# Kernel tuning notes

Hardware: AMD Instinct MI355X
Metric: run time of the kernel (lower is better)

## Reference

```python
import jax, jax.numpy as jnp
import numpy as np

N_NODES = 50000


def _gcn_conv(x, src, dst, W, b, n):
    # PyG GCNConv: h = x @ W; symmetric normalization with self-loops; scatter-add; + bias
    h = x @ W
    deg = jax.ops.segment_sum(jnp.ones_like(dst, dtype=h.dtype), dst, num_segments=n)
    dinv = jax.lax.rsqrt(jnp.maximum(deg, 1.0))  # self-loops guarantee deg >= 1
    norm = dinv[src] * dinv[dst]                 # [E_total]
    msgs = h[src] * norm[:, None]                # gather + scale
    out = jax.ops.segment_sum(msgs, dst, num_segments=n)
    return out + b


def setup_inputs() -> dict:
    key = jax.random.key(0)
    k1, k2, k3, k4 = jax.random.split(key, 4)
    d, f = 128, 128
    x = jax.random.normal(k1, (N_NODES, d), dtype=jnp.float32)
    edge_index = jax.random.randint(k2, (2, 800000), 0, N_NODES, dtype=jnp.int64)
    W1 = jax.random.normal(k3, (d, f), dtype=jnp.float32) / np.sqrt(d)
    b1 = jnp.zeros((f,), dtype=jnp.float32)
    W2 = jax.random.normal(k4, (f, 1), dtype=jnp.float32) / np.sqrt(f)
    b2 = jnp.zeros((1,), dtype=jnp.float32)
    return {"x": x, "edge_index": edge_index, "W1": W1, "b1": b1, "W2": W2, "b2": b2}


def reference(x, edge_index, W1, b1, W2, b2):
    n = x.shape[0]
    loops = jnp.arange(n, dtype=edge_index.dtype)
    src = jnp.concatenate([edge_index[0], loops])
    dst = jnp.concatenate([edge_index[1], loops])
    h = _gcn_conv(x, src, dst, W1, b1, n)
    h = jax.nn.relu(h)
    out = _gcn_conv(h, src, dst, W2, b2, n)
    return out
```

## Files before the change

### kernel.cpp

```cpp
#include <hip/hip_runtime.h>
#include <hip/hip_fp16.h>

#define D 128
#define BINW 128
#define BINCAP 4096
#define BINA_BLOCKS 512

typedef _Float16 half8 __attribute__((ext_vector_type(8)));
typedef float float4v __attribute__((ext_vector_type(4)));

__global__ void detect_kernel(const int* __restrict__ idx, int* __restrict__ flag) {
  if (threadIdx.x == 0 && blockIdx.x == 0) {
    int any = 0;
    for (int i = 0; i < 64; ++i) any |= idx[2 * i + 1];
    *flag = (any == 0) ? 1 : 0;
  }
}

__global__ __launch_bounds__(256) void bin_scatter_kernel(const int* __restrict__ idx,
                                                          const int* __restrict__ flagp,
                                                          int* __restrict__ binCount,
                                                          unsigned* __restrict__ binned,
                                                          int E, int nbin) {
  __shared__ int hist[512];
  __shared__ int cur[512];
  const int t = threadIdx.x;
  for (int b = t; b < 512; b += 256) hist[b] = 0;
  __syncthreads();
  const int is64 = *flagp;
  const int chunk = (E + gridDim.x - 1) / gridDim.x;
  const int lo = blockIdx.x * chunk;
  const int hi = min(lo + chunk, E);
  for (int e = lo + t; e < hi; e += 256) {
    int d = is64 ? idx[2 * (E + e)] : idx[E + e];
    atomicAdd(&hist[d >> 7], 1);
  }
  __syncthreads();
  for (int b = t; b < nbin; b += 256) {
    int hv = hist[b];
    cur[b] = hv ? atomicAdd(&binCount[b], hv) : 0;
  }
  __syncthreads();
  for (int e = lo + t; e < hi; e += 256) {
    int s, d;
    if (is64) { s = idx[2 * e]; d = idx[2 * (E + e)]; }
    else      { s = idx[e];     d = idx[E + e]; }
    int b = d >> 7;
    int pos = atomicAdd(&cur[b], 1);
    pos = min(pos, BINCAP - 1);
    binned[(size_t)b * BINCAP + pos] = (unsigned)s | ((unsigned)(d & 127) << 16);
  }
}

__global__ __launch_bounds__(256) void bin_sort_kernel(const int* __restrict__ binCount,
                                                       const unsigned* __restrict__ binned,
                                                       unsigned short* __restrict__ csr,
                                                       int* __restrict__ rowptr,
                                                       int* __restrict__ rend,
                                                       float* __restrict__ dinv,
                                                       int n, int nbin) {
  __shared__ unsigned rec[BINCAP];
  __shared__ unsigned short srt[BINCAP];
  __shared__ int hist[BINW];
  __shared__ int scn[BINW];
  __shared__ int cur[BINW];
  const int t = threadIdx.x;
  const int b = blockIdx.x;
  int cnt = binCount[b];
  if (cnt > BINCAP) cnt = BINCAP;
  const size_t gbase = (size_t)b * BINCAP;

  for (int i = t; i < cnt; i += 256) rec[i] = binned[gbase + i];
  if (t < BINW) hist[t] = 0;
  __syncthreads();
  for (int i = t; i < cnt; i += 256) atomicAdd(&hist[rec[i] >> 16], 1);
  __syncthreads();
  if (t < BINW) scn[t] = hist[t];
  __syncthreads();
  for (int off = 1; off < BINW; off <<= 1) {
    int u = 0;
    if (t < BINW && t >= off) u = scn[t - off];
    __syncthreads();
    if (t < BINW) scn[t] += u;
    __syncthreads();
  }
  if (t < BINW) cur[t] = scn[t] - hist[t];
  __syncthreads();
  for (int i = t; i < cnt; i += 256) {
    unsigned r = rec[i];
    int pos = atomicAdd(&cur[r >> 16], 1);
    srt[pos] = (unsigned short)(r & 0xFFFFu);
  }
  __syncthreads();
  const unsigned* srt32 = (const unsigned*)srt;
  unsigned* csr32 = (unsigned*)(csr + gbase);
  for (int i = t; i < (cnt + 1) / 2; i += 256) csr32[i] = srt32[i];

  const int node = b * BINW + t;
  if (t < BINW && node < n) {
    int deg = hist[t];
    int start = (int)gbase + (scn[t] - deg);
    rowptr[node] = start;
    rend[node]   = start + deg;
    dinv[node]   = rsqrtf((float)(deg + 1));
  }
}

__global__ __launch_bounds__(256) void gemm1_mfma_kernel(const float* __restrict__ x,
                                                         const float* __restrict__ W,
                                                         __half* __restrict__ h, int n) {
  __shared__ uint4 bfrag[8][4][64];
  const int t = threadIdx.x;

  for (int e = t; e < 2048; e += 256) {
    const int nt = e >> 8;
    const int kk = (e >> 6) & 3;
    const int L  = e & 63;
    const int nn = nt * 16 + (L & 15);
    const int k0 = kk * 32 + (L >> 4) * 8;
    half8 v;
#pragma unroll
    for (int j = 0; j < 8; ++j) v[j] = (_Float16)W[(k0 + j) * D + nn];
    bfrag[nt][kk][L] = *(uint4*)&v;
  }
  __syncthreads();

  const int wave = t >> 6;
  const int lane = t & 63;
  const int r0 = blockIdx.x * 64 + wave * 16;
  if (r0 >= n) return;

  const int mrow = r0 + (lane & 15);
  const int mc = (mrow < n) ? mrow : (n - 1);
  half8 af[4];
#pragma unroll
  for (int kk = 0; kk < 4; ++kk) {
    const float* xp = x + (size_t)mc * D + kk * 32 + (lane >> 4) * 8;
    float4 lo = *(const float4*)xp;
    float4 hi = *(const float4*)(xp + 4);
    half8 v;
    v[0] = (_Float16)lo.x; v[1] = (_Float16)lo.y;
    v[2] = (_Float16)lo.z; v[3] = (_Float16)lo.w;
    v[4] = (_Float16)hi.x; v[5] = (_Float16)hi.y;
    v[6] = (_Float16)hi.z; v[7] = (_Float16)hi.w;
    af[kk] = v;
  }

  float4v acc[8];
#pragma unroll
  for (int nt = 0; nt < 8; ++nt) acc[nt] = (float4v){0.f, 0.f, 0.f, 0.f};

#pragma unroll
  for (int nt = 0; nt < 8; ++nt) {
    uint4 b0 = bfrag[nt][0][lane];
    uint4 b1 = bfrag[nt][1][lane];
    uint4 b2 = bfrag[nt][2][lane];
    uint4 b3 = bfrag[nt][3][lane];
    acc[nt] = __builtin_amdgcn_mfma_f32_16x16x32_f16(af[0], *(half8*)&b0, acc[nt], 0, 0, 0);
    acc[nt] = __builtin_amdgcn_mfma_f32_16x16x32_f16(af[1], *(half8*)&b1, acc[nt], 0, 0, 0);
    acc[nt] = __builtin_amdgcn_mfma_f32_16x16x32_f16(af[2], *(half8*)&b2, acc[nt], 0, 0, 0);
    acc[nt] = __builtin_amdgcn_mfma_f32_16x16x32_f16(af[3], *(half8*)&b3, acc[nt], 0, 0, 0);
  }

  const int rbase = r0 + (lane >> 4) * 4;
  const int col = lane & 15;
#pragma unroll
  for (int r = 0; r < 4; ++r) {
    const int rr = rbase + r;
    if (rr < n) {
      __half* hp = h + (size_t)rr * D + col;
#pragma unroll
      for (int nt = 0; nt < 8; ++nt) hp[nt * 16] = __float2half(acc[nt][r]);
    }
  }
}

__device__ __forceinline__ void unpack8(uint4 p, float f[8]) {
  float2 t;
  t = __half22float2(*(__half2*)&p.x); f[0] = t.x; f[1] = t.y;
  t = __half22float2(*(__half2*)&p.y); f[2] = t.x; f[3] = t.y;
  t = __half22float2(*(__half2*)&p.z); f[4] = t.x; f[5] = t.y;
  t = __half22float2(*(__half2*)&p.w); f[6] = t.x; f[7] = t.y;
}

__global__ __launch_bounds__(256) void gather1_kernel(const __half* __restrict__ h,
                                                      const int* __restrict__ rowptr,
                                                      const int* __restrict__ rend,
                                                      const unsigned short* __restrict__ csr,
                                                      const float* __restrict__ dinv,
                                                      const float* __restrict__ b1,
                                                      const float* __restrict__ W2,
                                                      float* __restrict__ zw, int n) {
  const int node = blockIdx.x * 4 + (threadIdx.x >> 6);
  if (node >= n) return;
  const int lane = threadIdx.x & 63;
  const int q    = lane >> 4;
  const int fb   = (lane & 15) * 8;

  const float di = dinv[node];
  float a[8] = {0.f, 0.f, 0.f, 0.f, 0.f, 0.f, 0.f, 0.f};
  if (q == 0) {
    uint4 p = *(const uint4*)(h + (size_t)node * D + fb);
    float f[8]; unpack8(p, f);
    float s2 = di * di;
#pragma unroll
    for (int k = 0; k < 8; ++k) a[k] = f[k] * s2;
  }

  const int end = rend[node];
  int j = rowptr[node] + q;
  while (j + 4 < end) {
    int s0 = csr[j];
    int s1 = csr[j + 4];
    uint4 p0 = *(const uint4*)(h + (size_t)s0 * D + fb);
    uint4 p1 = *(const uint4*)(h + (size_t)s1 * D + fb);
    float w0 = di * dinv[s0];
    float w1 = di * dinv[s1];
    float f0[8], f1[8]; unpack8(p0, f0); unpack8(p1, f1);
#pragma unroll
    for (int k = 0; k < 8; ++k) a[k] = fmaf(f0[k], w0, a[k]);
#pragma unroll
    for (int k = 0; k < 8; ++k) a[k] = fmaf(f1[k], w1, a[k]);
    j += 8;
  }
  if (j < end) {
    int s0 = csr[j];
    uint4 p0 = *(const uint4*)(h + (size_t)s0 * D + fb);
    float w0 = di * dinv[s0];
    float f0[8]; unpack8(p0, f0);
#pragma unroll
    for (int k = 0; k < 8; ++k) a[k] = fmaf(f0[k], w0, a[k]);
  }

#pragma unroll
  for (int k = 0; k < 8; ++k) {
    a[k] += __shfl_xor(a[k], 16, 64);
    a[k] += __shfl_xor(a[k], 32, 64);
  }

  float4 blo = *(const float4*)(b1 + fb);
  float4 bhi = *(const float4*)(b1 + fb + 4);
  float4 wlo = *(const float4*)(W2 + fb);
  float4 whi = *(const float4*)(W2 + fb + 4);
  float bb[8] = {blo.x, blo.y, blo.z, blo.w, bhi.x, bhi.y, bhi.z, bhi.w};
  float ww[8] = {wlo.x, wlo.y, wlo.z, wlo.w, whi.x, whi.y, whi.z, whi.w};
  float p = 0.f;
#pragma unroll
  for (int k = 0; k < 8; ++k) p += fmaxf(a[k] + bb[k], 0.f) * ww[k];
#pragma unroll
  for (int off = 8; off > 0; off >>= 1) p += __shfl_xor(p, off, 64);
  if (lane == 0) zw[node] = p * di;
}

__global__ void gather2_kernel(const float* __restrict__ zw,
                               const float* __restrict__ dinv,
                               const int* __restrict__ rowptr,
                               const int* __restrict__ rend,
                               const unsigned short* __restrict__ csr,
                               const float* __restrict__ b2,
                               float* __restrict__ out, int n) {
  int i = blockIdx.x * blockDim.x + threadIdx.x;
  if (i >= n) return;
  float s = zw[i];
  const int lo = rowptr[i], hi = rend[i];
  for (int j = lo; j < hi; ++j) s += zw[csr[j]];
  out[i] = s * dinv[i] + b2[0];
}

extern "C" void kernel_launch(void* const* d_in, const int* in_sizes, int n_in,
                              void* d_out, int out_size, void* d_ws, size_t ws_size,
                              hipStream_t stream) {
  const float* x   = (const float*)d_in[0];
  const int*   idx = (const int*)d_in[1];
  const float* W1  = (const float*)d_in[2];
  const float* b1  = (const float*)d_in[3];
  const float* W2  = (const float*)d_in[4];
  const float* b2  = (const float*)d_in[5];
  float* out = (float*)d_out;

  const int n = in_sizes[0] / D;
  const int E = in_sizes[1] / 2;
  const int nbin = (n + BINW - 1) / BINW;

  char* ws = (char*)d_ws;
  size_t off = 0;
  auto carve = [&](size_t bytes) { char* p = ws + off; off += (bytes + 255) & ~(size_t)255; return p; };
  int*            flag     = (int*)carve(4);
  int*            binCount = (int*)carve((size_t)nbin * 4);
  unsigned*       binned   = (unsigned*)carve((size_t)nbin * BINCAP * 4);
  unsigned short* csr      = (unsigned short*)carve((size_t)nbin * BINCAP * 2);
  int*            rowptr   = (int*)carve((size_t)n * 4);
  int*            rend     = (int*)carve((size_t)n * 4);
  float*          dinv     = (float*)carve((size_t)n * 4);
  __half*         h        = (__half*)carve((size_t)n * D * 2);
  float*          zw       = (float*)carve((size_t)n * 4);

  detect_kernel<<<1, 64, 0, stream>>>(idx, flag);
  hipMemsetAsync(binCount, 0, (size_t)nbin * 4, stream);
  bin_scatter_kernel<<<BINA_BLOCKS, 256, 0, stream>>>(idx, flag, binCount, binned, E, nbin);
  bin_sort_kernel<<<nbin, 256, 0, stream>>>(binCount, binned, csr, rowptr, rend, dinv, n, nbin);
  gemm1_mfma_kernel<<<(n + 63) / 64, 256, 0, stream>>>(x, W1, h, n);
  gather1_kernel<<<(n + 3) / 4, 256, 0, stream>>>(h, rowptr, rend, csr, dinv, b1, W2, zw, n);
  gather2_kernel<<<(n + 255) / 256, 256, 0, stream>>>(zw, dinv, rowptr, rend, csr, b2, out, n);
}
```

Before: 161.5 us.

## Fold index-width detection into scatter, stage GEMM output, unroll gathers deeper

Removes the separate detect kernel launch: each scatter block now works out the int32/int64 index width itself by reading the first 64 entries. The GEMM stages its fp16 output tile through shared memory so global stores become coalesced 16-byte writes instead of scattered 2-byte ones. The layer-1 gather loop now issues four independent neighbor row loads per iteration instead of two, using predicated dummy loads for the tail. The layer-2 gather is unrolled by four. In exchange, every scatter block repeats the detection reads, the GEMM gains two barriers, and the gather uses more registers.

```diff
diff --git a/kernel.cpp b/kernel.cpp
--- a/kernel.cpp
+++ b/kernel.cpp
@@ -9,25 +9,22 @@
 typedef _Float16 half8 __attribute__((ext_vector_type(8)));
 typedef float float4v __attribute__((ext_vector_type(4)));
 
-__global__ void detect_kernel(const int* __restrict__ idx, int* __restrict__ flag) {
-  if (threadIdx.x == 0 && blockIdx.x == 0) {
-    int any = 0;
-    for (int i = 0; i < 64; ++i) any |= idx[2 * i + 1];
-    *flag = (any == 0) ? 1 : 0;
-  }
-}
-
 __global__ __launch_bounds__(256) void bin_scatter_kernel(const int* __restrict__ idx,
-                                                          const int* __restrict__ flagp,
                                                           int* __restrict__ binCount,
                                                           unsigned* __restrict__ binned,
                                                           int E, int nbin) {
   __shared__ int hist[512];
   __shared__ int cur[512];
+  __shared__ int s_is64;
   const int t = threadIdx.x;
   for (int b = t; b < 512; b += 256) hist[b] = 0;
-  __syncthreads();
-  const int is64 = *flagp;
+  if (t == 0) {
+    int any = 0;
+    for (int i = 0; i < 64; ++i) any |= idx[2 * i + 1];
+    s_is64 = (any == 0) ? 1 : 0;
+  }
+  __syncthreads();
+  const int is64 = s_is64;
   const int chunk = (E + gridDim.x - 1) / gridDim.x;
   const int lo = blockIdx.x * chunk;
   const int hi = min(lo + chunk, E);
@@ -109,7 +106,8 @@
 __global__ __launch_bounds__(256) void gemm1_mfma_kernel(const float* __restrict__ x,
                                                          const float* __restrict__ W,
                                                          __half* __restrict__ h, int n) {
-  __shared__ uint4 bfrag[8][4][64];
+  __shared__ uint4 smem[2048];
+  uint4 (*bfrag)[4][64] = (uint4(*)[4][64])smem;
   const int t = threadIdx.x;
 
   for (int e = t; e < 2048; e += 256) {
@@ -128,7 +126,6 @@
   const int wave = t >> 6;
   const int lane = t & 63;
   const int r0 = blockIdx.x * 64 + wave * 16;
-  if (r0 >= n) return;
 
   const int mrow = r0 + (lane & 15);
   const int mc = (mrow < n) ? mrow : (n - 1);
@@ -162,16 +159,25 @@
     acc[nt] = __builtin_amdgcn_mfma_f32_16x16x32_f16(af[3], *(half8*)&b3, acc[nt], 0, 0, 0);
   }
 
-  const int rbase = r0 + (lane >> 4) * 4;
-  const int col = lane & 15;
-#pragma unroll
-  for (int r = 0; r < 4; ++r) {
-    const int rr = rbase + r;
-    if (rr < n) {
-      __half* hp = h + (size_t)rr * D + col;
-#pragma unroll
-      for (int nt = 0; nt < 8; ++nt) hp[nt * 16] = __float2half(acc[nt][r]);
-    }
+  __syncthreads();
+  __half* hout = (__half*)smem;
+  const int quad = lane >> 4;
+  const int col  = lane & 15;
+  const int rloc = wave * 16 + quad * 4;
+#pragma unroll
+  for (int r = 0; r < 4; ++r)
+#pragma unroll
+    for (int nt = 0; nt < 8; ++nt)
+      hout[(rloc + r) * D + nt * 16 + col] = __float2half(acc[nt][r]);
+  __syncthreads();
+
+  const size_t rowbase = (size_t)blockIdx.x * 64;
+#pragma unroll
+  for (int i = 0; i < 4; ++i) {
+    const int elt = i * 256 + t;
+    const int rr  = elt >> 4;
+    if (rowbase + rr < (size_t)n)
+      *(uint4*)(h + (rowbase + rr) * D + (elt & 15) * 8) = smem[elt];
   }
 }
 
@@ -208,28 +214,31 @@
   }
 
   const int end = rend[node];
-  int j = rowptr[node] + q;
-  while (j + 4 < end) {
+  for (int j = rowptr[node] + q; j < end; j += 16) {
+    const int j1 = j + 4, j2 = j + 8, j3 = j + 12;
+    const bool v1 = j1 < end, v2 = j2 < end, v3 = j3 < end;
     int s0 = csr[j];
-    int s1 = csr[j + 4];
+    int s1 = v1 ? csr[j1] : s0;
+    int s2 = v2 ? csr[j2] : s0;
+    int s3 = v3 ? csr[j3] : s0;
     uint4 p0 = *(const uint4*)(h + (size_t)s0 * D + fb);
     uint4 p1 = *(const uint4*)(h + (size_t)s1 * D + fb);
+    uint4 p2 = *(const uint4*)(h + (size_t)s2 * D + fb);
+    uint4 p3 = *(const uint4*)(h + (size_t)s3 * D + fb);
     float w0 = di * dinv[s0];
-    float w1 = di * dinv[s1];
-    float f0[8], f1[8]; unpack8(p0, f0); unpack8(p1, f1);
+    float w1 = v1 ? di * dinv[s1] : 0.f;
+    float w2 = v2 ? di * dinv[s2] : 0.f;
+    float w3 = v3 ? di * dinv[s3] : 0.f;
+    float f0[8], f1[8], f2[8], f3[8];
+    unpack8(p0, f0); unpack8(p1, f1); unpack8(p2, f2); unpack8(p3, f3);
 #pragma unroll
     for (int k = 0; k < 8; ++k) a[k] = fmaf(f0[k], w0, a[k]);
 #pragma unroll
     for (int k = 0; k < 8; ++k) a[k] = fmaf(f1[k], w1, a[k]);
-    j += 8;
-  }
-  if (j < end) {
-    int s0 = csr[j];
-    uint4 p0 = *(const uint4*)(h + (size_t)s0 * D + fb);
-    float w0 = di * dinv[s0];
-    float f0[8]; unpack8(p0, f0);
-#pragma unroll
-    for (int k = 0; k < 8; ++k) a[k] = fmaf(f0[k], w0, a[k]);
+#pragma unroll
+    for (int k = 0; k < 8; ++k) a[k] = fmaf(f2[k], w2, a[k]);
+#pragma unroll
+    for (int k = 0; k < 8; ++k) a[k] = fmaf(f3[k], w3, a[k]);
   }
 
 #pragma unroll
@@ -263,7 +272,12 @@
   if (i >= n) return;
   float s = zw[i];
   const int lo = rowptr[i], hi = rend[i];
-  for (int j = lo; j < hi; ++j) s += zw[csr[j]];
+  int j = lo;
+  for (; j + 4 <= hi; j += 4) {
+    int a0 = csr[j], a1 = csr[j + 1], a2 = csr[j + 2], a3 = csr[j + 3];
+    s += zw[a0] + zw[a1] + zw[a2] + zw[a3];
+  }
+  for (; j < hi; ++j) s += zw[csr[j]];
   out[i] = s * dinv[i] + b2[0];
 }
 
@@ -285,7 +299,6 @@
   char* ws = (char*)d_ws;
   size_t off = 0;
   auto carve = [&](size_t bytes) { char* p = ws + off; off += (bytes + 255) & ~(size_t)255; return p; };
-  int*            flag     = (int*)carve(4);
   int*            binCount = (int*)carve((size_t)nbin * 4);
   unsigned*       binned   = (unsigned*)carve((size_t)nbin * BINCAP * 4);
   unsigned short* csr      = (unsigned short*)carve((size_t)nbin * BINCAP * 2);
@@ -295,9 +308,8 @@
   __half*         h        = (__half*)carve((size_t)n * D * 2);
   float*          zw       = (float*)carve((size_t)n * 4);
 
-  detect_kernel<<<1, 64, 0, stream>>>(idx, flag);
   hipMemsetAsync(binCount, 0, (size_t)nbin * 4, stream);
-  bin_scatter_kernel<<<BINA_BLOCKS, 256, 0, stream>>>(idx, flag, binCount, binned, E, nbin);
+  bin_scatter_kernel<<<BINA_BLOCKS, 256, 0, stream>>>(idx, binCount, binned, E, nbin);
   bin_sort_kernel<<<nbin, 256, 0, stream>>>(binCount, binned, csr, rowptr, rend, dinv, n, nbin);
   gemm1_mfma_kernel<<<(n + 63) / 64, 256, 0, stream>>>(x, W1, h, n);
   gather1_kernel<<<(n + 3) / 4, 256, 0, stream>>>(h, rowptr, rend, csr, dinv, b1, W2, zw, n);
```

New measurement: 158.0 us. -2.2%, faster.
